# Kernel tuning notes

Hardware: AMD Instinct MI355X
Metric: run time of the kernel (lower is better)

The kernel has to match this reference:

```python
import jax, jax.numpy as jnp
import numpy as np

TEMPERATURE = 8.0  # sqrt(d_k) with d_k = 64
NEG_INF = -1e30    # finite stand-in for -inf; exp() underflows to 0 identically


def _skew(s):
    # Music-Transformer relative-position skew: F.pad(s,(1,0)).view(-1,L+1,L)[:,1:,:]
    B, L, _ = s.shape
    s = jnp.pad(s, ((0, 0), (0, 0), (1, 0)))  # [B, L, L+1]
    return s.reshape(B, L + 1, L)[:, 1:, :]   # [B, L, L]


def setup_inputs() -> dict:
    key = jax.random.key(0)
    kq, kk, kv, ke = jax.random.split(key, 4)
    B, L, D = 16, 2048, 64
    q = jax.random.normal(kq, (B, L, D), dtype=jnp.float32)
    k = jax.random.normal(kk, (B, L, D), dtype=jnp.float32)
    v = jax.random.normal(kv, (B, L, D), dtype=jnp.float32)
    e = jax.random.normal(ke, (B, L, D), dtype=jnp.float32)
    # causal mask (True = masked out), broadcast to batch
    mask = jnp.broadcast_to(jnp.triu(jnp.ones((L, L), dtype=bool), k=1), (B, L, L))
    return {"q": q, "k": k, "v": v, "e": e, "mask": mask}


def reference(q, k, v, e, mask):
    attn = jnp.einsum('bqd,bkd->bqk', q, k)          # q @ k^T
    attn = attn + _skew(jnp.einsum('bqd,bkd->bqk', q, e))
    attn = attn / TEMPERATURE
    attn = jnp.where(mask, NEG_INF, attn)
    attn = jax.nn.softmax(attn, axis=2)
    attn = jnp.where(mask, 0.0, attn)
    # dropout is identity in eval mode
    output = jnp.einsum('bqk,bkd->bqd', attn, v)
    return (output, attn)
```

## Files before the change

### kernel.cpp

```cpp
#include <hip/hip_runtime.h>

typedef unsigned int u32;
typedef __fp16 h2 __attribute__((ext_vector_type(2)));
typedef _Float16 f16x8 __attribute__((ext_vector_type(8)));
typedef float f32x4 __attribute__((ext_vector_type(4)));

#define BB 16
#define LL 2048
#define DD 64
#define RPB 16
#define NTHREADS 256
#define NBLK (LL / RPB)

union U32H2 { u32 u; h2 h; };
__device__ __forceinline__ u32 as_u32(h2 x) { U32H2 t; t.h = x; return t.u; }

__device__ __forceinline__ h2 pk(float x, float y) {
#if __has_builtin(__builtin_amdgcn_cvt_pkrtz)
    return __builtin_amdgcn_cvt_pkrtz(x, y);
#else
    h2 r; r.x = (__fp16)x; r.y = (__fp16)y; return r;
#endif
}

__device__ __forceinline__ float fdot2f(u32 a, u32 b, float c) {
#if __has_builtin(__builtin_amdgcn_fdot2)
    U32H2 ta; ta.u = a; U32H2 tb; tb.u = b;
    return __builtin_amdgcn_fdot2(ta.h, tb.h, c, false);
#else
    U32H2 ta; ta.u = a; U32H2 tb; tb.u = b;
    c = fmaf((float)ta.h.x, (float)tb.h.x, c);
    return fmaf((float)ta.h.y, (float)tb.h.y, c);
#endif
}

union F8U { f16x8 v; h2 p[4]; };
__device__ __forceinline__ f16x8 pack8(float4 a, float4 b) {
    F8U u;
    u.p[0] = pk(a.x, a.y); u.p[1] = pk(a.z, a.w);
    u.p[2] = pk(b.x, b.y); u.p[3] = pk(b.z, b.w);
    return u.v;
}

#define MFMA(A, B, C) __builtin_amdgcn_mfma_f32_16x16x32_f16((A), (B), (C), 0, 0, 0)

__global__ __launch_bounds__(NTHREADS, 2) void attn_fused(
    const float* __restrict__ qg, const float* __restrict__ kg,
    const float* __restrict__ vg, const float* __restrict__ eg,
    float* __restrict__ out_o, float* __restrict__ out_attn)
{
    __shared__ __fp16 S_h[RPB][LL];
    __shared__ float  G_scr[4][RPB][34];
    __shared__ float  maxbuf[RPB][64];
    __shared__ float  linv[RPB];

    const int tid  = threadIdx.x;
    const int wave = tid >> 6;
    const int lane = tid & 63;
    const int o4   = lane >> 4;
    const int lc   = lane & 15;
    const int b    = blockIdx.x / NBLK;
    const int r0   = (blockIdx.x % NBLK) * RPB;
    const int nT   = (r0 >> 6) + 1;

    const float* qb = qg + (size_t)b * LL * DD;
    const float* kb = kg + (size_t)b * LL * DD;
    const float* eb = eg + (size_t)b * LL * DD;
    const float* vb = vg + (size_t)b * LL * DD;

    f16x8 qa0, qa1;
    {
        const float* qr = qb + (size_t)(r0 + lc) * DD + 8 * o4;
        float4 a0 = *(const float4*)(qr);
        float4 a1 = *(const float4*)(qr + 4);
        float4 b0 = *(const float4*)(qr + 32);
        float4 b1 = *(const float4*)(qr + 36);
        qa0 = pack8(a0, a1);
        qa1 = pack8(b0, b1);
    }

    float mx[4] = {-60000.f, -60000.f, -60000.f, -60000.f};
    float* Gp = &G_scr[wave][0][0];

    const int span = r0 + 15 - (wave << 4);
    const int nTw  = (span >= 0) ? ((span >> 6) + 1) : 0;

    for (int t = 0; t < nTw; ++t) {
        const int c0w = (t << 6) + (wave << 4);

        const float* kr = kb + (size_t)(c0w + lc) * DD + 8 * o4;
        float4 k0 = *(const float4*)(kr);
        float4 k1 = *(const float4*)(kr + 4);
        float4 k2 = *(const float4*)(kr + 32);
        float4 k3 = *(const float4*)(kr + 36);

        const int j0w = c0w + 2032 - r0;
        int er0 = j0w + lc;      if (er0 > LL - 1) er0 = LL - 1;
        int er1 = j0w + 16 + lc; if (er1 > LL - 1) er1 = LL - 1;
        const float* e0p = eb + (size_t)er0 * DD + 8 * o4;
        const float* e1p = eb + (size_t)er1 * DD + 8 * o4;
        float4 ea0 = *(const float4*)(e0p);
        float4 ea1 = *(const float4*)(e0p + 4);
        float4 ea2 = *(const float4*)(e0p + 32);
        float4 ea3 = *(const float4*)(e0p + 36);
        float4 eb0 = *(const float4*)(e1p);
        float4 eb1 = *(const float4*)(e1p + 4);
        float4 eb2 = *(const float4*)(e1p + 32);
        float4 eb3 = *(const float4*)(e1p + 36);

        f16x8 kf0 = pack8(k0, k1), kf1 = pack8(k2, k3);
        f16x8 ef00 = pack8(ea0, ea1), ef01 = pack8(ea2, ea3);
        f16x8 ef10 = pack8(eb0, eb1), ef11 = pack8(eb2, eb3);

        const f32x4 z = {0.f, 0.f, 0.f, 0.f};
        f32x4 dk = MFMA(qa0, kf0, z);  dk = MFMA(qa1, kf1, dk);
        f32x4 g0 = MFMA(qa0, ef00, z); g0 = MFMA(qa1, ef01, g0);
        f32x4 g1 = MFMA(qa0, ef10, z); g1 = MFMA(qa1, ef11, g1);

#pragma unroll
        for (int i = 0; i < 4; ++i) {
            Gp[(4 * o4 + i) * 34 + lc]      = g0[i];
            Gp[(4 * o4 + i) * 34 + 16 + lc] = g1[i];
        }
#pragma unroll
        for (int i = 0; i < 4; ++i) {
            const int rl = 4 * o4 + i;
            const int lj = lc - rl + 15;
            float s = (dk[i] + Gp[rl * 34 + lj]) * 0.125f;
            const int c = c0w + lc;
            if (c > r0 + rl) s = -60000.f;
            mx[i] = fmaxf(mx[i], s);
            S_h[rl][c] = (__fp16)s;
        }
    }

#pragma unroll
    for (int i = 0; i < 4; ++i)
        maxbuf[4 * o4 + i][(wave << 4) + lc] = mx[i];
    __syncthreads();

    for (int ri2 = 0; ri2 < 4; ++ri2) {
        const int rl = (wave << 2) + ri2;
        const int r  = r0 + rl;
        float m = maxbuf[rl][lane];
#pragma unroll
        for (int off = 32; off; off >>= 1) m = fmaxf(m, __shfl_xor(m, off, 64));
        float l = 0.f;
        for (int t = 0; t < nT; ++t) {
            const int c = (t << 6) + lane;
            float p = (c <= r) ? __expf((float)S_h[rl][c] - m) : 0.f;
            l += p;
            S_h[rl][c] = (__fp16)p;
        }
#pragma unroll
        for (int off = 32; off; off >>= 1) l += __shfl_xor(l, off, 64);
        const float inv = 1.f / l;
        if (lane == 0) linv[rl] = inv;
        float* arow = out_attn + ((size_t)b * LL + r) * LL;
#pragma unroll 4
        for (int t = 0; t < LL / 64; ++t) {
            const int c = (t << 6) + lane;
            arow[c] = (c <= r) ? (float)S_h[rl][c] * inv : 0.f;
        }
    }
    __syncthreads();

    float o[16];
#pragma unroll
    for (int i = 0; i < 16; ++i) o[i] = 0.f;

    for (int t = wave; t < nT; t += 4) {
#pragma unroll
        for (int ch = 0; ch < 8; ++ch) {
            const int cb = (t << 6) + (ch << 3);
            const float* vp = vb + (size_t)cb * DD + lane;
            float v0 = vp[0],      v1 = vp[DD],     v2 = vp[2*DD], v3 = vp[3*DD];
            float v4 = vp[4*DD],   v5 = vp[5*DD],   v6 = vp[6*DD], v7 = vp[7*DD];
            u32 vv0 = as_u32(pk(v0, v1)), vv1 = as_u32(pk(v2, v3));
            u32 vv2 = as_u32(pk(v4, v5)), vv3 = as_u32(pk(v6, v7));
#pragma unroll
            for (int ri = 0; ri < 16; ++ri) {
                uint4 pq = *(const uint4*)&S_h[ri][cb];
                o[ri] = fdot2f(pq.x, vv0, o[ri]);
                o[ri] = fdot2f(pq.y, vv1, o[ri]);
                o[ri] = fdot2f(pq.z, vv2, o[ri]);
                o[ri] = fdot2f(pq.w, vv3, o[ri]);
            }
        }
    }
    __syncthreads();

    float* ored = (float*)S_h;
#pragma unroll
    for (int ri = 0; ri < 16; ++ri) ored[(wave * 16 + ri) * 64 + lane] = o[ri];
    __syncthreads();

#pragma unroll
    for (int j = 0; j < 4; ++j) {
        const int i  = tid + j * 256;
        const int ri = i >> 6, d = i & 63;
        float s = ored[(0 * 16 + ri) * 64 + d] + ored[(1 * 16 + ri) * 64 + d]
                + ored[(2 * 16 + ri) * 64 + d] + ored[(3 * 16 + ri) * 64 + d];
        out_o[((size_t)b * LL + r0 + ri) * DD + d] = s * linv[ri];
    }
}

extern "C" void kernel_launch(void* const* d_in, const int* in_sizes, int n_in,
                              void* d_out, int out_size, void* d_ws, size_t ws_size,
                              hipStream_t stream) {
    const float* q = (const float*)d_in[0];
    const float* k = (const float*)d_in[1];
    const float* v = (const float*)d_in[2];
    const float* e = (const float*)d_in[3];
    float* out_o    = (float*)d_out;
    float* out_attn = out_o + (size_t)BB * LL * DD;

    dim3 grid(BB * NBLK);
    attn_fused<<<grid, NTHREADS, 0, stream>>>(q, k, v, e, out_o, out_attn);
}
```

Before: 780.1 us.

## Use MFMA for P·V, shuffle-based skew, swizzled LDS and 512-thread blocks

Replaces the fdot2-based P·V accumulation with 16x16x32 f16 MFMA tiles read from a shared score buffer. The buffer uses an XOR column swizzle to cut LDS bank conflicts. The relative-position skew is now done with wave shuffles instead of an LDS scratch round-trip. Blocks grow to 8 waves: the QK tiling stride becomes 128 columns, softmax takes 2 rows per wave, and a two-half reduction combines the output. Risks include register pressure from launch_bounds(512,4) and extra shuffle instructions.

New measurement: 651.6 us. 1.2x faster.

```diff
diff --git a/kernel.cpp b/kernel.cpp
--- a/kernel.cpp
+++ b/kernel.cpp
@@ -9,11 +9,8 @@
 #define LL 2048
 #define DD 64
 #define RPB 16
-#define NTHREADS 256
+#define NTHREADS 512
 #define NBLK (LL / RPB)
-
-union U32H2 { u32 u; h2 h; };
-__device__ __forceinline__ u32 as_u32(h2 x) { U32H2 t; t.h = x; return t.u; }
 
 __device__ __forceinline__ h2 pk(float x, float y) {
 #if __has_builtin(__builtin_amdgcn_cvt_pkrtz)
@@ -23,17 +20,6 @@
 #endif
 }
 
-__device__ __forceinline__ float fdot2f(u32 a, u32 b, float c) {
-#if __has_builtin(__builtin_amdgcn_fdot2)
-    U32H2 ta; ta.u = a; U32H2 tb; tb.u = b;
-    return __builtin_amdgcn_fdot2(ta.h, tb.h, c, false);
-#else
-    U32H2 ta; ta.u = a; U32H2 tb; tb.u = b;
-    c = fmaf((float)ta.h.x, (float)tb.h.x, c);
-    return fmaf((float)ta.h.y, (float)tb.h.y, c);
-#endif
-}
-
 union F8U { f16x8 v; h2 p[4]; };
 __device__ __forceinline__ f16x8 pack8(float4 a, float4 b) {
     F8U u;
@@ -44,14 +30,15 @@
 
 #define MFMA(A, B, C) __builtin_amdgcn_mfma_f32_16x16x32_f16((A), (B), (C), 0, 0, 0)
 
-__global__ __launch_bounds__(NTHREADS, 2) void attn_fused(
+__device__ __forceinline__ int swc(int rl, int c) { return c ^ ((rl & 7) << 3); }
+
+__global__ __launch_bounds__(NTHREADS, 4) void attn_fused(
     const float* __restrict__ qg, const float* __restrict__ kg,
     const float* __restrict__ vg, const float* __restrict__ eg,
     float* __restrict__ out_o, float* __restrict__ out_attn)
 {
     __shared__ __fp16 S_h[RPB][LL];
-    __shared__ float  G_scr[4][RPB][34];
-    __shared__ float  maxbuf[RPB][64];
+    __shared__ float  maxF[RPB][132];
     __shared__ float  linv[RPB];
 
     const int tid  = threadIdx.x;
@@ -80,13 +67,12 @@
     }
 
     float mx[4] = {-60000.f, -60000.f, -60000.f, -60000.f};
-    float* Gp = &G_scr[wave][0][0];
 
     const int span = r0 + 15 - (wave << 4);
-    const int nTw  = (span >= 0) ? ((span >> 6) + 1) : 0;
+    const int nTw  = (span >= 0) ? ((span >> 7) + 1) : 0;
 
     for (int t = 0; t < nTw; ++t) {
-        const int c0w = (t << 6) + (wave << 4);
+        const int c0w = (t << 7) + (wave << 4);
 
         const float* kr = kb + (size_t)(c0w + lc) * DD + 8 * o4;
         float4 k0 = *(const float4*)(kr);
@@ -119,38 +105,38 @@
 
 #pragma unroll
         for (int i = 0; i < 4; ++i) {
-            Gp[(4 * o4 + i) * 34 + lc]      = g0[i];
-            Gp[(4 * o4 + i) * 34 + 16 + lc] = g1[i];
-        }
-#pragma unroll
-        for (int i = 0; i < 4; ++i) {
-            const int rl = 4 * o4 + i;
-            const int lj = lc - rl + 15;
-            float s = (dk[i] + Gp[rl * 34 + lj]) * 0.125f;
+            const int rl  = 4 * o4 + i;
+            const int lj  = lc + 15 - rl;
+            const int src = (o4 << 4) | (lj & 15);
+            float ga = __shfl(g0[i], src, 64);
+            float gb = __shfl(g1[i], src, 64);
+            float gv = (lj < 16) ? ga : gb;
+            float s = (dk[i] + gv) * 0.125f;
             const int c = c0w + lc;
             if (c > r0 + rl) s = -60000.f;
             mx[i] = fmaxf(mx[i], s);
-            S_h[rl][c] = (__fp16)s;
+            S_h[rl][swc(rl, c)] = (__fp16)s;
         }
     }
 
 #pragma unroll
     for (int i = 0; i < 4; ++i)
-        maxbuf[4 * o4 + i][(wave << 4) + lc] = mx[i];
+        maxF[4 * o4 + i][(wave << 4) | lc] = mx[i];
     __syncthreads();
 
-    for (int ri2 = 0; ri2 < 4; ++ri2) {
-        const int rl = (wave << 2) + ri2;
+    for (int rr = 0; rr < 2; ++rr) {
+        const int rl = (wave << 1) + rr;
         const int r  = r0 + rl;
-        float m = maxbuf[rl][lane];
+        float m = fmaxf(maxF[rl][lane], maxF[rl][64 + lane]);
 #pragma unroll
         for (int off = 32; off; off >>= 1) m = fmaxf(m, __shfl_xor(m, off, 64));
         float l = 0.f;
         for (int t = 0; t < nT; ++t) {
-            const int c = (t << 6) + lane;
-            float p = (c <= r) ? __expf((float)S_h[rl][c] - m) : 0.f;
+            const int c  = (t << 6) + lane;
+            const int cs = swc(rl, c);
+            float p = (c <= r) ? __expf((float)S_h[rl][cs] - m) : 0.f;
             l += p;
-            S_h[rl][c] = (__fp16)p;
+            S_h[rl][cs] = (__fp16)p;
         }
 #pragma unroll
         for (int off = 32; off; off >>= 1) l += __shfl_xor(l, off, 64);
@@ -160,48 +146,46 @@
 #pragma unroll 4
         for (int t = 0; t < LL / 64; ++t) {
             const int c = (t << 6) + lane;
-            arow[c] = (c <= r) ? (float)S_h[rl][c] * inv : 0.f;
+            arow[c] = (c <= r) ? (float)S_h[rl][swc(rl, c)] * inv : 0.f;
         }
     }
     __syncthreads();
 
-    float o[16];
-#pragma unroll
-    for (int i = 0; i < 16; ++i) o[i] = 0.f;
-
-    for (int t = wave; t < nT; t += 4) {
-#pragma unroll
-        for (int ch = 0; ch < 8; ++ch) {
-            const int cb = (t << 6) + (ch << 3);
-            const float* vp = vb + (size_t)cb * DD + lane;
-            float v0 = vp[0],      v1 = vp[DD],     v2 = vp[2*DD], v3 = vp[3*DD];
-            float v4 = vp[4*DD],   v5 = vp[5*DD],   v6 = vp[6*DD], v7 = vp[7*DD];
-            u32 vv0 = as_u32(pk(v0, v1)), vv1 = as_u32(pk(v2, v3));
-            u32 vv2 = as_u32(pk(v4, v5)), vv3 = as_u32(pk(v6, v7));
-#pragma unroll
-            for (int ri = 0; ri < 16; ++ri) {
-                uint4 pq = *(const uint4*)&S_h[ri][cb];
-                o[ri] = fdot2f(pq.x, vv0, o[ri]);
-                o[ri] = fdot2f(pq.y, vv1, o[ri]);
-                o[ri] = fdot2f(pq.z, vv2, o[ri]);
-                o[ri] = fdot2f(pq.w, vv3, o[ri]);
-            }
-        }
+    const int dw = (wave & 3) << 4;
+    const int th = wave >> 2;
+    f32x4 acc = {0.f, 0.f, 0.f, 0.f};
+    const int koff = o4 << 3;
+
+    for (int t = th; t < nT; t += 2) {
+        const int cb = t << 6;
+        f16x8 pa0 = *(const f16x8*)&S_h[lc][swc(lc, cb + koff)];
+        f16x8 pa1 = *(const f16x8*)&S_h[lc][swc(lc, cb + 32 + koff)];
+        const float* vp0 = vb + (size_t)(cb + koff) * DD + dw + lc;
+        const float* vp1 = vb + (size_t)(cb + 32 + koff) * DD + dw + lc;
+        float a0 = vp0[0],      a1 = vp0[DD],     a2 = vp0[2*DD], a3 = vp0[3*DD];
+        float a4 = vp0[4*DD],   a5 = vp0[5*DD],   a6 = vp0[6*DD], a7 = vp0[7*DD];
+        float c0 = vp1[0],      c1 = vp1[DD],     c2 = vp1[2*DD], c3 = vp1[3*DD];
+        float c4 = vp1[4*DD],   c5 = vp1[5*DD],   c6 = vp1[6*DD], c7 = vp1[7*DD];
+        f16x8 vf0 = pack8(make_float4(a0, a1, a2, a3), make_float4(a4, a5, a6, a7));
+        f16x8 vf1 = pack8(make_float4(c0, c1, c2, c3), make_float4(c4, c5, c6, c7));
+        acc = MFMA(pa0, vf0, acc);
+        acc = MFMA(pa1, vf1, acc);
+    }
+
+    float* red = &maxF[0][0];
+    if (wave >= 4) {
+#pragma unroll
+        for (int i = 0; i < 4; ++i)
+            red[(wave & 3) * 256 + (4 * o4 + i) * 16 + lc] = acc[i];
     }
     __syncthreads();
-
-    float* ored = (float*)S_h;
-#pragma unroll
-    for (int ri = 0; ri < 16; ++ri) ored[(wave * 16 + ri) * 64 + lane] = o[ri];
-    __syncthreads();
-
-#pragma unroll
-    for (int j = 0; j < 4; ++j) {
-        const int i  = tid + j * 256;
-        const int ri = i >> 6, d = i & 63;
-        float s = ored[(0 * 16 + ri) * 64 + d] + ored[(1 * 16 + ri) * 64 + d]
-                + ored[(2 * 16 + ri) * 64 + d] + ored[(3 * 16 + ri) * 64 + d];
-        out_o[((size_t)b * LL + r0 + ri) * DD + d] = s * linv[ri];
+    if (wave < 4) {
+#pragma unroll
+        for (int i = 0; i < 4; ++i) {
+            const int rl = 4 * o4 + i;
+            float oo = acc[i] + red[wave * 256 + rl * 16 + lc];
+            out_o[((size_t)b * LL + r0 + rl) * DD + dw + lc] = oo * linv[rl];
+        }
     }
 }
 
```
